# Performance work log

Measured on AMD Instinct MI355X. Metric: run time of the kernel, lower is better.

## Reference

```python
import jax, jax.numpy as jnp
import numpy as np

B, T, C, H = 4, 1024, 1024, 16
D = C // H
EPS = 1e-5


def _ln(x, g, b):
    mu = jnp.mean(x, axis=-1, keepdims=True)
    var = jnp.mean((x - mu) ** 2, axis=-1, keepdims=True)
    return (x - mu) * jax.lax.rsqrt(var + EPS) * g + b


def _attn(xq, xkv, wq, wk, wv, wo, bo, mask):
    # wq/wk/wv/wo: [C, C] (in, out). Dropout is identity in eval mode.
    Bq, Tq, _ = xq.shape
    Tk = xkv.shape[1]
    q = (xq @ wq).reshape(Bq, Tq, H, D)
    k = (xkv @ wk).reshape(Bq, Tk, H, D)
    v = (xkv @ wv).reshape(Bq, Tk, H, D)
    scores = jnp.einsum('bqhd,bkhd->bhqk', q, k) / jnp.sqrt(jnp.float32(D))
    if mask is not None:
        scores = jnp.where(mask == 0, -jnp.inf, scores)
    p = jax.nn.softmax(scores, axis=-1)
    out = jnp.einsum('bhqk,bkhd->bqhd', p, v).reshape(Bq, Tq, C)
    return out @ wo + bo


def setup_inputs() -> dict:
    key = jax.random.key(0)
    ks = jax.random.split(key, 20)
    s = 0.02
    inp = {
        'x': jax.random.normal(ks[0], (B, T, C), jnp.float32),
        'encoder_out': jax.random.normal(ks[1], (B, T, C), jnp.float32),
        'sa_wq': jax.random.normal(ks[2], (C, C), jnp.float32) * s,
        'sa_wk': jax.random.normal(ks[3], (C, C), jnp.float32) * s,
        'sa_wv': jax.random.normal(ks[4], (C, C), jnp.float32) * s,
        'sa_wo': jax.random.normal(ks[5], (C, C), jnp.float32) * s,
        'sa_bo': jnp.zeros((C,), jnp.float32),
        'ca_wq': jax.random.normal(ks[6], (C, C), jnp.float32) * s,
        'ca_wk': jax.random.normal(ks[7], (C, C), jnp.float32) * s,
        'ca_wv': jax.random.normal(ks[8], (C, C), jnp.float32) * s,
        'ca_wo': jax.random.normal(ks[9], (C, C), jnp.float32) * s,
        'ca_bo': jnp.zeros((C,), jnp.float32),
        'ff_w1': jax.random.normal(ks[10], (C, 4 * C), jnp.float32) * s,
        'ff_b1': jnp.zeros((4 * C,), jnp.float32),
        'ff_w2': jax.random.normal(ks[11], (4 * C, C), jnp.float32) * s,
        'ff_b2': jnp.zeros((C,), jnp.float32),
        'ln1_g': jnp.ones((C,), jnp.float32), 'ln1_b': jnp.zeros((C,), jnp.float32),
        'ln2_g': jnp.ones((C,), jnp.float32), 'ln2_b': jnp.zeros((C,), jnp.float32),
        'ln3_g': jnp.ones((C,), jnp.float32), 'ln3_b': jnp.zeros((C,), jnp.float32),
        'tgt_mask': jnp.tril(jnp.ones((T, T), jnp.int32))[None, None],  # [1,1,T,T] causal
        'src_mask': jnp.ones((B, 1, 1, T), jnp.int32),
    }
    return inp


def reference(x, encoder_out, sa_wq, sa_wk, sa_wv, sa_wo, sa_bo,
              ca_wq, ca_wk, ca_wv, ca_wo, ca_bo,
              ff_w1, ff_b1, ff_w2, ff_b2,
              ln1_g, ln1_b, ln2_g, ln2_b, ln3_g, ln3_b,
              tgt_mask, src_mask):
    # self-attention (masked) + residual
    x = x + _attn(_ln(x, ln1_g, ln1_b), _ln(x, ln1_g, ln1_b),
                  sa_wq, sa_wk, sa_wv, sa_wo, sa_bo, tgt_mask)
    # cross-attention + residual (only src_mask applied to scores)
    h = _ln(x, ln2_g, ln2_b)
    x = x + _attn(h, encoder_out, ca_wq, ca_wk, ca_wv, ca_wo, ca_bo, src_mask)
    # FFN + residual
    h = _ln(x, ln3_g, ln3_b)
    x = x + (jax.nn.relu(h @ ff_w1 + ff_b1) @ ff_w2 + ff_b2)
    return x
```

## Files before the change

kernel.cpp:

```cpp
#include <hip/hip_runtime.h>

typedef __bf16 bf16_t;
typedef __bf16 bf16x4 __attribute__((ext_vector_type(4)));
typedef __bf16 bf16x8 __attribute__((ext_vector_type(8)));
typedef float  f32x4  __attribute__((ext_vector_type(4)));

#define LN_EPS 1e-5f

__device__ __forceinline__ void g2l16(const bf16_t* g, bf16_t* l) {
    __builtin_amdgcn_global_load_lds(
        (const __attribute__((address_space(1))) void*)g,
        (__attribute__((address_space(3))) void*)l, 16, 0, 0);
}

__global__ __launch_bounds__(256) void cvt_kernel(
    const float* __restrict__ x, bf16_t* __restrict__ y)
{
    int i = blockIdx.x * 256 + threadIdx.x;
    f32x4 v = ((const f32x4*)x)[i];
    bf16x4 o = { (bf16_t)v.x, (bf16_t)v.y, (bf16_t)v.z, (bf16_t)v.w };
    ((bf16x4*)y)[i] = o;
}

struct WT16 {
    const float* src[16]; bf16_t* dst[16];
    int srcN[16]; int dstK[16]; int k0b[16]; int n0b[16];
};

__global__ __launch_bounds__(256) void wt16_kernel(WT16 p)
{
    const int z = blockIdx.z;
    const float* W = p.src[z];
    bf16_t* Wt = p.dst[z];
    const int N = p.srcN[z], Kd = p.dstK[z];
    const int n0 = p.n0b[z] + blockIdx.x * 64, k0 = p.k0b[z] + blockIdx.y * 64;
    __shared__ float ts[64][65];
    const int tid = threadIdx.x;
#pragma unroll
    for (int it = 0; it < 4; ++it) {
        int f = tid + it * 256;
        int row = f >> 4, c4 = (f & 15) * 4;
        f32x4 v = *(const f32x4*)(W + (size_t)(k0 + row) * N + n0 + c4);
        ts[row][c4 + 0] = v.x; ts[row][c4 + 1] = v.y;
        ts[row][c4 + 2] = v.z; ts[row][c4 + 3] = v.w;
    }
    __syncthreads();
#pragma unroll
    for (int it = 0; it < 4; ++it) {
        int f = tid + it * 256;
        int nrow = f >> 4, k4 = (f & 15) * 4;
        bf16x4 o = { (bf16_t)ts[k4 + 0][nrow], (bf16_t)ts[k4 + 1][nrow],
                     (bf16_t)ts[k4 + 2][nrow], (bf16_t)ts[k4 + 3][nrow] };
        *(bf16x4*)(Wt + (size_t)(n0 + nrow) * Kd + k0 + k4) = o;
    }
}

__global__ __launch_bounds__(256) void ln_kernel(
    const float* __restrict__ x, const float* __restrict__ g,
    const float* __restrict__ b, bf16_t* __restrict__ y)
{
    const int row = blockIdx.x;
    const int tid = threadIdx.x;
    const f32x4* xr = (const f32x4*)(x + (size_t)row * 1024);
    f32x4 v = xr[tid];
    float s  = v.x + v.y + v.z + v.w;
    float s2 = v.x*v.x + v.y*v.y + v.z*v.z + v.w*v.w;
#pragma unroll
    for (int off = 1; off < 64; off <<= 1) {
        s  += __shfl_xor(s,  off, 64);
        s2 += __shfl_xor(s2, off, 64);
    }
    __shared__ float ws_[4], ws2_[4];
    const int wave = tid >> 6, lane = tid & 63;
    if (lane == 0) { ws_[wave] = s; ws2_[wave] = s2; }
    __syncthreads();
    s  = ws_[0] + ws_[1] + ws_[2] + ws_[3];
    s2 = ws2_[0] + ws2_[1] + ws2_[2] + ws2_[3];
    const float mu   = s  * (1.0f/1024.0f);
    const float var  = s2 * (1.0f/1024.0f) - mu*mu;
    const float rstd = rsqrtf(var + LN_EPS);
    f32x4 gv = ((const f32x4*)g)[tid];
    f32x4 bv = ((const f32x4*)b)[tid];
    f32x4 o  = (v - mu) * rstd * gv + bv;
    bf16x4 ob = { (bf16_t)o.x, (bf16_t)o.y, (bf16_t)o.z, (bf16_t)o.w };
    ((bf16x4*)(y + (size_t)row * 1024))[tid] = ob;
}

template<int BN, int DEPTH, int OUT_BF16, int HAS_BIAS, int DO_RELU, int HAS_RES>
__global__ __launch_bounds__(256) void gemm_bf16(
    const bf16_t* __restrict__ A, const bf16_t* __restrict__ Bt,
    const float* __restrict__ bias, const float* __restrict__ res,
    void* __restrict__ out, int M, int N, int K)
{
    constexpr int NT = BN / 32;
    __shared__ __align__(16) bf16_t As[2][DEPTH][128 * 32];
    __shared__ __align__(16) bf16_t Bs[2][DEPTH][BN * 32];

    const int tid  = threadIdx.x;
    const int wave = tid >> 6, lane = tid & 63;
    const int q    = lane >> 4, r = lane & 15;
    const int wm   = wave >> 1, wn = wave & 1;

    const int nbx  = gridDim.x;
    const int id   = blockIdx.y * nbx + blockIdx.x;
    const int mper = gridDim.y >> 3;
    const int jj   = id >> 3;
    const int bm   = (id & 7) * mper + jj / nbx;
    const int bn   = jj % nbx;
    const int m0   = bm * 128, n0 = bn * BN;

    const int srow = lane >> 2;
    const int schk = ((lane & 3) ^ ((lane >> 3) & 3)) * 8;
    const int rsw  = ((r >> 1) & 3) * 8;

    auto stage = [&](int buf, int kk) {
#pragma unroll
        for (int s = 0; s < DEPTH; ++s) {
#pragma unroll
            for (int t = 0; t < 2; ++t) {
                int rowA = wave * 32 + t * 16;
                g2l16(A + (size_t)(m0 + rowA + srow) * K + kk + s * 32 + schk,
                      &As[buf][s][rowA * 32]);
            }
#pragma unroll
            for (int t = 0; t < BN / 64; ++t) {
                int rowB = wave * (BN / 4) + t * 16;
                g2l16(Bt + (size_t)(n0 + rowB + srow) * K + kk + s * 32 + schk,
                      &Bs[buf][s][rowB * 32]);
            }
        }
    };

    f32x4 acc[4][NT] = {};
    constexpr int STEP = 32 * DEPTH;
    stage(0, 0);

    for (int kk = 0; kk < K; kk += STEP) {
        const int cur = (kk / STEP) & 1;
        __syncthreads();
        if (kk + STEP < K) stage(cur ^ 1, kk + STEP);
#pragma unroll
        for (int s = 0; s < DEPTH; ++s) {
            bf16x8 af[4], bfr[NT];
#pragma unroll
            for (int i = 0; i < 4; ++i)
                af[i] = *(const bf16x8*)&As[cur][s][(wm * 64 + i * 16 + r) * 32 + (q * 8 ^ rsw)];
#pragma unroll
            for (int j = 0; j < NT; ++j)
                bfr[j] = *(const bf16x8*)&Bs[cur][s][(wn * 16 * NT + j * 16 + r) * 32 + (q * 8 ^ rsw)];
#pragma unroll
            for (int i = 0; i < 4; ++i)
#pragma unroll
                for (int j = 0; j < NT; ++j)
                    acc[i][j] = __builtin_amdgcn_mfma_f32_16x16x32_bf16(af[i], bfr[j], acc[i][j], 0, 0, 0);
        }
    }

#pragma unroll
    for (int i = 0; i < 4; ++i)
#pragma unroll
        for (int j = 0; j < NT; ++j)
#pragma unroll
            for (int e = 0; e < 4; ++e) {
                int row = m0 + wm * 64 + i * 16 + q * 4 + e;
                int col = n0 + wn * 16 * NT + j * 16 + r;
                float v = acc[i][j][e];
                if (HAS_BIAS) v += bias[col];
                if (DO_RELU)  v = v > 0.0f ? v : 0.0f;
                if (HAS_RES)  v += res[(size_t)row * N + col];
                if (OUT_BF16) ((bf16_t*)out)[(size_t)row * N + col] = (bf16_t)v;
                else          ((float*)out)[(size_t)row * N + col] = v;
            }
}

__global__ __launch_bounds__(256) void gemm_qkv3(
    const bf16_t* __restrict__ Aq, const bf16_t* __restrict__ Akv,
    const bf16_t* __restrict__ Wt3,
    bf16_t* __restrict__ outq, bf16_t* __restrict__ outk,
    bf16_t* __restrict__ vt)
{
    const int K = 1024;
    __shared__ __align__(16) bf16_t As[2][128 * 32];
    __shared__ __align__(16) bf16_t Bs[2][128 * 32];

    const int tid  = threadIdx.x;
    const int wave = tid >> 6, lane = tid & 63;
    const int q    = lane >> 4, r = lane & 15;
    const int wm   = wave >> 1, wn = wave & 1;

    const int nbx  = gridDim.x;
    const int id   = blockIdx.y * nbx + blockIdx.x;
    const int mper = gridDim.y >> 3;
    const int jj   = id >> 3;
    const int bm   = (id & 7) * mper + jj / nbx;
    const int bn   = jj % nbx;
    const int m0   = bm * 128, n0 = bn * 128;
    const int grp  = bn >> 3;
    const bf16_t* A = (grp == 0) ? Aq : Akv;

    const int srow = lane >> 2;
    const int schk = ((lane & 3) ^ ((lane >> 3) & 3)) * 8;
    const int rsw  = ((r >> 1) & 3) * 8;

    auto stage = [&](int buf, int kk) {
#pragma unroll
        for (int t = 0; t < 2; ++t) {
            int row = wave * 32 + t * 16;
            g2l16(A   + (size_t)(m0 + row + srow) * K + kk + schk, &As[buf][row * 32]);
            g2l16(Wt3 + (size_t)(n0 + row + srow) * K + kk + schk, &Bs[buf][row * 32]);
        }
    };

    f32x4 acc[4][4] = {};
    stage(0, 0);

    for (int kk = 0; kk < K; kk += 32) {
        const int cur = (kk >> 5) & 1;
        __syncthreads();
        if (kk + 32 < K) stage(cur ^ 1, kk + 32);

        bf16x8 af[4], bfr[4];
#pragma unroll
        for (int i = 0; i < 4; ++i)
            af[i] = *(const bf16x8*)&As[cur][(wm * 64 + i * 16 + r) * 32 + (q * 8 ^ rsw)];
#pragma unroll
        for (int j = 0; j < 4; ++j)
            bfr[j] = *(const bf16x8*)&Bs[cur][(wn * 64 + j * 16 + r) * 32 + (q * 8 ^ rsw)];
#pragma unroll
        for (int i = 0; i < 4; ++i)
#pragma unroll
            for (int j = 0; j < 4; ++j)
                acc[i][j] = __builtin_amdgcn_mfma_f32_16x16x32_bf16(af[i], bfr[j], acc[i][j], 0, 0, 0);
    }

    if (grp < 2) {
        bf16_t* o = (grp == 0) ? outq : outk;
        const float sc = (grp == 0) ? 0.125f : 1.0f;
        const int c0 = n0 - grp * 1024;
#pragma unroll
        for (int i = 0; i < 4; ++i)
#pragma unroll
            for (int j = 0; j < 4; ++j)
#pragma unroll
                for (int e = 0; e < 4; ++e) {
                    int row = m0 + wm * 64 + i * 16 + q * 4 + e;
                    int col = c0 + wn * 64 + j * 16 + r;
                    o[(size_t)row * 1024 + col] = (bf16_t)(acc[i][j][e] * sc);
                }
    } else {
#pragma unroll
        for (int i = 0; i < 4; ++i)
#pragma unroll
            for (int j = 0; j < 4; ++j) {
                int c = (n0 - 2048) + wn * 64 + j * 16 + r;
                int hh = c >> 6, d = c & 63;
                int row0 = m0 + wm * 64 + i * 16 + q * 4;
                int bb = row0 >> 10, t = row0 & 1023;
                bf16x4 pk = { (bf16_t)acc[i][j][0], (bf16_t)acc[i][j][1],
                              (bf16_t)acc[i][j][2], (bf16_t)acc[i][j][3] };
                *(bf16x4*)&vt[((size_t)((bb << 4) + hh) * 64 + d) * 1024 + t] = pk;
            }
    }
}

template<int CAUSAL>
__global__ __launch_bounds__(256) void attn_mfma_kernel(
    const bf16_t* __restrict__ Qp, const bf16_t* __restrict__ Kp,
    const bf16_t* __restrict__ VTp, bf16_t* __restrict__ Op)
{
    const int T = 1024;
    const int LP = 72;
    __shared__ __align__(16) bf16_t Ps[128 * LP];
    __shared__ __align__(16) bf16_t Ks[2][2][64 * 32];
    __shared__ __align__(16) bf16_t Vs[2][2][64 * 32];

    const int id  = blockIdx.x + 8 * (blockIdx.y + 16 * blockIdx.z);
    int pr, qt;
    if (CAUSAL) {
        const int lo = id & 255;
        pr = lo >> 2;
        const int qp = lo & 3;
        qt = (id >= 256) ? (7 - qp) : qp;
    } else {
        const int jj = id >> 3;
        pr = (id & 7) * 8 + (jj >> 3);
        qt = jj & 7;
    }
    const int h   = pr & 15, b = pr >> 4;

    const int tid  = threadIdx.x;
    const int wave = tid >> 6, lane = tid & 63;
    const int q    = lane >> 4, r = lane & 15;
    const int srow = lane >> 2;
    const int schk = ((lane & 3) ^ ((lane >> 3) & 3)) * 8;
    const int rsw  = ((r >> 1) & 3) * 8;

    const bf16_t* Kb = Kp + (size_t)(b * T) * 1024 + h * 64;
    const bf16_t* Vb = VTp + (size_t)((b * 16 + h) * 64) * 1024;

    auto stageKV = [&](int buf, int kt) {
#pragma unroll
        for (int ks = 0; ks < 2; ++ks) {
            g2l16(Kb + (size_t)(kt * 64 + wave * 16 + srow) * 1024 + ks * 32 + schk,
                  &Ks[buf][ks][wave * 16 * 32]);
            g2l16(Vb + (size_t)(wave * 16 + srow) * 1024 + kt * 64 + ks * 32 + schk,
                  &Vs[buf][ks][wave * 16 * 32]);
        }
    };

    {
        const bf16_t* Qb = Qp + (size_t)(b * T + qt * 128) * 1024 + h * 64;
#pragma unroll
        for (int it = 0; it < 4; ++it) {
            int f = tid + it * 256;
            int row = f >> 3, c8 = (f & 7) * 8;
            *(bf16x8*)&Ps[row * LP + c8] = *(const bf16x8*)(Qb + (size_t)row * 1024 + c8);
        }
    }
    __syncthreads();
    bf16x8 qa[2][2];
#pragma unroll
    for (int mt = 0; mt < 2; ++mt)
#pragma unroll
        for (int ks = 0; ks < 2; ++ks)
            qa[mt][ks] = *(const bf16x8*)&Ps[(wave * 32 + mt * 16 + r) * LP + ks * 32 + q * 8];

    const bf16_t one_b = (bf16_t)1.0f;
    const bf16x8 ones = { one_b, one_b, one_b, one_b, one_b, one_b, one_b, one_b };

    f32x4 o[2][4] = {};
    f32x4 ol[2] = {};

    const int nk = CAUSAL ? (2 * qt + 2) : 16;
    stageKV(0, 0);

    for (int kt = 0; kt < nk; ++kt) {
        const int cur = kt & 1;
        __syncthreads();
        if (kt + 1 < nk) stageKV(cur ^ 1, kt + 1);

        f32x4 s[2][4] = {};
#pragma unroll
        for (int ks = 0; ks < 2; ++ks)
#pragma unroll
            for (int nt = 0; nt < 4; ++nt) {
                bf16x8 kb = *(const bf16x8*)&Ks[cur][ks][(nt * 16 + r) * 32 + (q * 8 ^ rsw)];
#pragma unroll
                for (int mt = 0; mt < 2; ++mt)
                    s[mt][nt] = __builtin_amdgcn_mfma_f32_16x16x32_bf16(qa[mt][ks], kb, s[mt][nt], 0, 0, 0);
            }

        if (CAUSAL) {
#pragma unroll
            for (int mt = 0; mt < 2; ++mt) {
                const int r0 = qt * 128 + wave * 32 + mt * 16;
                if (kt * 64 + 63 > r0) {
#pragma unroll
                    for (int nt = 0; nt < 4; ++nt) {
                        int kg = kt * 64 + nt * 16 + r;
#pragma unroll
                        for (int i2 = 0; i2 < 4; ++i2)
                            if (kg > r0 + q * 4 + i2) s[mt][nt][i2] = -INFINITY;
                    }
                }
            }
        }

#pragma unroll
        for (int mt = 0; mt < 2; ++mt)
#pragma unroll
            for (int nt = 0; nt < 4; ++nt)
#pragma unroll
                for (int i2 = 0; i2 < 4; ++i2)
                    Ps[(wave * 32 + mt * 16 + q * 4 + i2) * LP + nt * 16 + r] =
                        (bf16_t)__expf(s[mt][nt][i2]);

#pragma unroll
        for (int ks = 0; ks < 2; ++ks) {
            bf16x8 pa[2];
#pragma unroll
            for (int mt = 0; mt < 2; ++mt)
                pa[mt] = *(const bf16x8*)&Ps[(wave * 32 + mt * 16 + r) * LP + ks * 32 + q * 8];
#pragma unroll
            for (int dt = 0; dt < 4; ++dt) {
                bf16x8 vb = *(const bf16x8*)&Vs[cur][ks][(dt * 16 + r) * 32 + (q * 8 ^ rsw)];
#pragma unroll
                for (int mt = 0; mt < 2; ++mt)
                    o[mt][dt] = __builtin_amdgcn_mfma_f32_16x16x32_bf16(pa[mt], vb, o[mt][dt], 0, 0, 0);
            }
#pragma unroll
            for (int mt = 0; mt < 2; ++mt)
                ol[mt] = __builtin_amdgcn_mfma_f32_16x16x32_bf16(pa[mt], ones, ol[mt], 0, 0, 0);
        }
    }

    bf16_t* Ob = Op + (size_t)(b * T + qt * 128 + wave * 32) * 1024 + h * 64;
#pragma unroll
    for (int mt = 0; mt < 2; ++mt) {
        f32x4 inv;
#pragma unroll
        for (int i2 = 0; i2 < 4; ++i2) inv[i2] = 1.0f / ol[mt][i2];
#pragma unroll
        for (int dt = 0; dt < 4; ++dt)
#pragma unroll
            for (int i2 = 0; i2 < 4; ++i2)
                Ob[(size_t)(mt * 16 + q * 4 + i2) * 1024 + dt * 16 + r] = (bf16_t)(o[mt][dt][i2] * inv[i2]);
    }
}

extern "C" void kernel_launch(void* const* d_in, const int* in_sizes, int n_in,
                              void* d_out, int out_size, void* d_ws, size_t ws_size,
                              hipStream_t stream)
{
    const float* x     = (const float*)d_in[0];
    const float* enc   = (const float*)d_in[1];
    const float* sa_wq = (const float*)d_in[2];
    const float* sa_wk = (const float*)d_in[3];
    const float* sa_wv = (const float*)d_in[4];
    const float* sa_wo = (const float*)d_in[5];
    const float* sa_bo = (const float*)d_in[6];
    const float* ca_wq = (const float*)d_in[7];
    const float* ca_wk = (const float*)d_in[8];
    const float* ca_wv = (const float*)d_in[9];
    const float* ca_wo = (const float*)d_in[10];
    const float* ca_bo = (const float*)d_in[11];
    const float* ff_w1 = (const float*)d_in[12];
    const float* ff_b1 = (const float*)d_in[13];
    const float* ff_w2 = (const float*)d_in[14];
    const float* ff_b2 = (const float*)d_in[15];
    const float* ln1_g = (const float*)d_in[16];
    const float* ln1_b = (const float*)d_in[17];
    const float* ln2_g = (const float*)d_in[18];
    const float* ln2_b = (const float*)d_in[19];
    const float* ln3_g = (const float*)d_in[20];
    const float* ln3_b = (const float*)d_in[21];

    float* out = (float*)d_out;
    char* ws = (char*)d_ws;
    const size_t MB = 1024 * 1024;
    bf16_t* w_s3  = (bf16_t*)(ws +  0 * MB);
    bf16_t* w_so  = (bf16_t*)(ws +  6 * MB);
    bf16_t* w_c3  = (bf16_t*)(ws +  8 * MB);
    bf16_t* w_co  = (bf16_t*)(ws + 14 * MB);
    bf16_t* w_f1  = (bf16_t*)(ws + 16 * MB);
    bf16_t* w_f2  = (bf16_t*)(ws + 24 * MB);
    bf16_t* b_enc = (bf16_t*)(ws + 32 * MB);
    bf16_t* b_ln  = (bf16_t*)(ws + 40 * MB);
    bf16_t* b_q   = (bf16_t*)(ws + 48 * MB);
    bf16_t* b_k   = (bf16_t*)(ws + 56 * MB);
    bf16_t* b_vt  = (bf16_t*)(ws + 64 * MB);
    bf16_t* b_at  = (bf16_t*)(ws + 72 * MB);
    float*  b_x1  = (float*) (ws + 80 * MB);
    float*  b_x2  = (float*) (ws + 48 * MB);
    bf16_t* b_h1  = (bf16_t*)(ws + 64 * MB);

    const int M = 4096;
    dim3 blk(256);

    WT16 wp;
    const float* srcs[8] = { sa_wq, sa_wk, sa_wv, sa_wo, ca_wq, ca_wk, ca_wv, ca_wo };
    bf16_t* dsts[8] = { w_s3, w_s3 + 1024*1024, w_s3 + 2048*1024, w_so,
                        w_c3, w_c3 + 1024*1024, w_c3 + 2048*1024, w_co };
    for (int z = 0; z < 8; ++z) {
        wp.src[z] = srcs[z]; wp.dst[z] = dsts[z];
        wp.srcN[z] = 1024; wp.dstK[z] = 1024; wp.k0b[z] = 0; wp.n0b[z] = 0;
    }
    for (int z = 8; z < 12; ++z) {
        wp.src[z] = ff_w1; wp.dst[z] = w_f1;
        wp.srcN[z] = 4096; wp.dstK[z] = 1024; wp.k0b[z] = 0; wp.n0b[z] = (z - 8) * 1024;
    }
    for (int z = 12; z < 16; ++z) {
        wp.src[z] = ff_w2; wp.dst[z] = w_f2;
        wp.srcN[z] = 1024; wp.dstK[z] = 4096; wp.k0b[z] = (z - 12) * 1024; wp.n0b[z] = 0;
    }
    wt16_kernel<<<dim3(16, 16, 16), blk, 0, stream>>>(wp);
    cvt_kernel<<<4096, blk, 0, stream>>>(enc, b_enc);

    ln_kernel<<<4096, blk, 0, stream>>>(x, ln1_g, ln1_b, b_ln);
    gemm_qkv3<<<dim3(24, 32), blk, 0, stream>>>(b_ln, b_ln, w_s3, b_q, b_k, b_vt);
    attn_mfma_kernel<1><<<dim3(8, 16, 4), blk, 0, stream>>>(b_q, b_k, b_vt, b_at);
    gemm_bf16<64,2,0,1,0,1><<<dim3(16, 32), blk, 0, stream>>>(
        b_at, w_so, sa_bo, x, b_x1, M, 1024, 1024);
    ln_kernel<<<4096, blk, 0, stream>>>(b_x1, ln2_g, ln2_b, b_ln);
    gemm_qkv3<<<dim3(24, 32), blk, 0, stream>>>(b_ln, b_enc, w_c3, b_q, b_k, b_vt);
    attn_mfma_kernel<0><<<dim3(8, 16, 4), blk, 0, stream>>>(b_q, b_k, b_vt, b_at);
    gemm_bf16<64,2,0,1,0,1><<<dim3(16, 32), blk, 0, stream>>>(
        b_at, w_co, ca_bo, b_x1, b_x2, M, 1024, 1024);
    ln_kernel<<<4096, blk, 0, stream>>>(b_x2, ln3_g, ln3_b, b_ln);
    gemm_bf16<128,1,1,1,1,0><<<dim3(32, 32), blk, 0, stream>>>(
        b_ln, w_f1, ff_b1, nullptr, b_h1, M, 4096, 1024);
    gemm_bf16<64,2,0,1,0,1><<<dim3(16, 32), blk, 0, stream>>>(
        b_h1, w_f2, ff_b2, b_x2, out, M, 1024, 4096);
}
```

Before: 475.2 us.

## Add triple-buffered LDS pipeline with explicit vmcnt waits to BN=64 GEMMs

Adds an NBUF template parameter to the bf16 GEMM. With three buffers, loads are issued two stages ahead, and each iteration waits with an explicit s_waitcnt vmcnt(L) plus a raw barrier instead of __syncthreads. The goal is to keep more global-to-LDS loads in flight and hide memory latency in the output-projection and FFN2 GEMMs. It raises LDS use per block, which may lower occupancy, and it depends on the hand-set vmcnt counts being correct.

```diff
diff --git a/kernel.cpp b/kernel.cpp
--- a/kernel.cpp
+++ b/kernel.cpp
@@ -11,6 +11,21 @@
     __builtin_amdgcn_global_load_lds(
         (const __attribute__((address_space(1))) void*)g,
         (__attribute__((address_space(3))) void*)l, 16, 0, 0);
+}
+
+template<int N> __device__ __forceinline__ void wait_vm() {
+    if constexpr (N == 0)       asm volatile("s_waitcnt vmcnt(0)" ::: "memory");
+    else if constexpr (N == 2)  asm volatile("s_waitcnt vmcnt(2)" ::: "memory");
+    else if constexpr (N == 3)  asm volatile("s_waitcnt vmcnt(3)" ::: "memory");
+    else if constexpr (N == 4)  asm volatile("s_waitcnt vmcnt(4)" ::: "memory");
+    else if constexpr (N == 6)  asm volatile("s_waitcnt vmcnt(6)" ::: "memory");
+    else if constexpr (N == 8)  asm volatile("s_waitcnt vmcnt(8)" ::: "memory");
+    else if constexpr (N == 12) asm volatile("s_waitcnt vmcnt(12)" ::: "memory");
+    else                        asm volatile("s_waitcnt vmcnt(0)" ::: "memory");
+}
+__device__ __forceinline__ void block_bar() {
+    __builtin_amdgcn_s_barrier();
+    asm volatile("" ::: "memory");
 }
 
 __global__ __launch_bounds__(256) void cvt_kernel(
@@ -86,15 +101,17 @@
     ((bf16x4*)(y + (size_t)row * 1024))[tid] = ob;
 }
 
-template<int BN, int DEPTH, int OUT_BF16, int HAS_BIAS, int DO_RELU, int HAS_RES>
+template<int BN, int DEPTH, int NBUF, int OUT_BF16, int HAS_BIAS, int DO_RELU,
+         int HAS_RES>
 __global__ __launch_bounds__(256) void gemm_bf16(
     const bf16_t* __restrict__ A, const bf16_t* __restrict__ Bt,
     const float* __restrict__ bias, const float* __restrict__ res,
     void* __restrict__ out, int M, int N, int K)
 {
     constexpr int NT = BN / 32;
-    __shared__ __align__(16) bf16_t As[2][DEPTH][128 * 32];
-    __shared__ __align__(16) bf16_t Bs[2][DEPTH][BN * 32];
+    constexpr int L  = DEPTH * (2 + BN / 64);
+    __shared__ __align__(16) bf16_t As[NBUF][DEPTH][128 * 32];
+    __shared__ __align__(16) bf16_t Bs[NBUF][DEPTH][BN * 32];
 
     const int tid  = threadIdx.x;
     const int wave = tid >> 6, lane = tid & 63;
@@ -133,27 +150,45 @@
 
     f32x4 acc[4][NT] = {};
     constexpr int STEP = 32 * DEPTH;
-    stage(0, 0);
-
-    for (int kk = 0; kk < K; kk += STEP) {
-        const int cur = (kk / STEP) & 1;
-        __syncthreads();
-        if (kk + STEP < K) stage(cur ^ 1, kk + STEP);
+
+    auto compute = [&](int buf) {
 #pragma unroll
         for (int s = 0; s < DEPTH; ++s) {
             bf16x8 af[4], bfr[NT];
 #pragma unroll
             for (int i = 0; i < 4; ++i)
-                af[i] = *(const bf16x8*)&As[cur][s][(wm * 64 + i * 16 + r) * 32 + (q * 8 ^ rsw)];
+                af[i] = *(const bf16x8*)&As[buf][s][(wm * 64 + i * 16 + r) * 32 + (q * 8 ^ rsw)];
 #pragma unroll
             for (int j = 0; j < NT; ++j)
-                bfr[j] = *(const bf16x8*)&Bs[cur][s][(wn * 16 * NT + j * 16 + r) * 32 + (q * 8 ^ rsw)];
+                bfr[j] = *(const bf16x8*)&Bs[buf][s][(wn * 16 * NT + j * 16 + r) * 32 + (q * 8 ^ rsw)];
 #pragma unroll
             for (int i = 0; i < 4; ++i)
 #pragma unroll
                 for (int j = 0; j < NT; ++j)
                     acc[i][j] = __builtin_amdgcn_mfma_f32_16x16x32_bf16(af[i], bfr[j], acc[i][j], 0, 0, 0);
         }
+    };
+
+    if constexpr (NBUF == 2) {
+        stage(0, 0);
+        for (int kk = 0; kk < K; kk += STEP) {
+            const int cur = (kk / STEP) & 1;
+            __syncthreads();
+            if (kk + STEP < K) stage(cur ^ 1, kk + STEP);
+            compute(cur);
+        }
+    } else {
+        const int NK = K / STEP;
+        stage(0, 0); stage(1, STEP);
+        int t = 0;
+        for (; t + 2 < NK; ++t) {
+            wait_vm<L>();
+            block_bar();
+            stage((t + 2) % NBUF, (t + 2) * STEP);
+            compute(t % NBUF);
+        }
+        wait_vm<L>();  block_bar(); compute(t % NBUF); ++t;
+        wait_vm<0>();  block_bar(); compute(t % NBUF);
     }
 
 #pragma unroll
@@ -479,16 +514,16 @@
     ln_kernel<<<4096, blk, 0, stream>>>(x, ln1_g, ln1_b, b_ln);
     gemm_qkv3<<<dim3(24, 32), blk, 0, stream>>>(b_ln, b_ln, w_s3, b_q, b_k, b_vt);
     attn_mfma_kernel<1><<<dim3(8, 16, 4), blk, 0, stream>>>(b_q, b_k, b_vt, b_at);
-    gemm_bf16<64,2,0,1,0,1><<<dim3(16, 32), blk, 0, stream>>>(
+    gemm_bf16<64,2,3,0,1,0,1><<<dim3(16, 32), blk, 0, stream>>>(
         b_at, w_so, sa_bo, x, b_x1, M, 1024, 1024);
     ln_kernel<<<4096, blk, 0, stream>>>(b_x1, ln2_g, ln2_b, b_ln);
     gemm_qkv3<<<dim3(24, 32), blk, 0, stream>>>(b_ln, b_enc, w_c3, b_q, b_k, b_vt);
     attn_mfma_kernel<0><<<dim3(8, 16, 4), blk, 0, stream>>>(b_q, b_k, b_vt, b_at);
-    gemm_bf16<64,2,0,1,0,1><<<dim3(16, 32), blk, 0, stream>>>(
+    gemm_bf16<64,2,3,0,1,0,1><<<dim3(16, 32), blk, 0, stream>>>(
         b_at, w_co, ca_bo, b_x1, b_x2, M, 1024, 1024);
     ln_kernel<<<4096, blk, 0, stream>>>(b_x2, ln3_g, ln3_b, b_ln);
-    gemm_bf16<128,1,1,1,1,0><<<dim3(32, 32), blk, 0, stream>>>(
+    gemm_bf16<128,1,2,1,1,1,0><<<dim3(32, 32), blk, 0, stream>>>(
         b_ln, w_f1, ff_b1, nullptr, b_h1, M, 4096, 1024);
-    gemm_bf16<64,2,0,1,0,1><<<dim3(16, 32), blk, 0, stream>>>(
+    gemm_bf16<64,2,3,0,1,0,1><<<dim3(16, 32), blk, 0, stream>>>(
         b_h1, w_f2, ff_b2, b_x2, out, M, 1024, 4096);
 }
```

New measurement: 498.2 us. 4.9% more time.

## Add 256x256-tile 512-thread GEMM with quadrant pipelining for FFN up-projection

Applied to the files above, without the earlier changes.

Replaces the 128-tile FFN1 GEMM (bias+ReLU, bf16 out) with a new kernel that computes 256x256 output tiles using 8 waves, K-step 64, XOR-swizzled LDS and double buffering. Each K step is split into four quadrant phases that interleave async global-to-LDS loads of the next tile with MFMA work, using s_setprio and barriers, and block IDs are remapped for L2 locality. Larger tiles raise arithmetic intensity and cut global traffic, but the kernel uses 128KB of LDS and many accumulator registers, so occupancy is one block per CU. The grid is only 256 blocks.

```diff
diff --git a/kernel.cpp b/kernel.cpp
--- a/kernel.cpp
+++ b/kernel.cpp
@@ -171,6 +171,128 @@
                 if (OUT_BF16) ((bf16_t*)out)[(size_t)row * N + col] = (bf16_t)v;
                 else          ((float*)out)[(size_t)row * N + col] = v;
             }
+}
+
+__global__ __launch_bounds__(512) void gemm_256(
+    const bf16_t* __restrict__ A, const bf16_t* __restrict__ Bt,
+    const float* __restrict__ bias, bf16_t* __restrict__ out,
+    int M, int N, int K)
+{
+    __shared__ __align__(16) bf16_t lds[2][2][2][128 * 64];
+
+    const int tid  = threadIdx.x;
+    const int wave = tid >> 6, lane = tid & 63;
+    const int q    = lane >> 4, r = lane & 15;
+    const int wm   = wave >> 2, wn = wave & 3;
+
+    const int id  = blockIdx.y * gridDim.x + blockIdx.x;
+    const int sid = (id & 7) * 32 + (id >> 3);
+    const int bm  = sid >> 4, bn = sid & 15;
+    const int m0  = bm * 256, n0 = bn * 256;
+
+    int srow[2], selem[2];
+#pragma unroll
+    for (int l = 0; l < 2; ++l) {
+        int o  = (wave * 64 + lane) * 16 + l * 8192;
+        int lo = o ^ (((o >> 7) & 7) << 4);
+        srow[l]  = lo >> 7;
+        selem[l] = (lo & 127) >> 1;
+    }
+    const int sd0 = wave * 512;
+
+    auto stageA = [&](int buf, int h, int kt) {
+#pragma unroll
+        for (int l = 0; l < 2; ++l)
+            g2l16(A + (size_t)(m0 + h * 128 + srow[l]) * K + kt * 64 + selem[l],
+                  &lds[buf][0][h][sd0 + l * 4096]);
+    };
+    auto stageB = [&](int buf, int h, int kt) {
+#pragma unroll
+        for (int l = 0; l < 2; ++l)
+            g2l16(Bt + (size_t)(n0 + h * 128 + srow[l]) * K + kt * 64 + selem[l],
+                  &lds[buf][1][h][sd0 + l * 4096]);
+    };
+
+    int aoff[4][2], boff[2][2];
+#pragma unroll
+    for (int i = 0; i < 4; ++i) {
+        int row = wm * 64 + i * 16 + r;
+#pragma unroll
+        for (int ks = 0; ks < 2; ++ks) {
+            int colB = ks * 64 + q * 16;
+            aoff[i][ks] = (row * 128 + (colB ^ ((row & 7) << 4))) >> 1;
+        }
+    }
+#pragma unroll
+    for (int j = 0; j < 2; ++j) {
+        int row = wn * 32 + j * 16 + r;
+#pragma unroll
+        for (int ks = 0; ks < 2; ++ks) {
+            int colB = ks * 64 + q * 16;
+            boff[j][ks] = (row * 128 + (colB ^ ((row & 7) << 4))) >> 1;
+        }
+    }
+
+    f32x4 acc[2][2][4][2] = {};
+
+    stageA(0, 0, 0); stageB(0, 0, 0); stageB(0, 1, 0); stageA(0, 1, 0);
+    asm volatile("s_waitcnt vmcnt(0)" ::: "memory");
+    __builtin_amdgcn_s_barrier();
+    asm volatile("" ::: "memory");
+
+    const int NTk = K >> 6;
+
+#define QPHASE(HA, HB, STMT_STAGE, VMC_ST, VMC_LAST)                           \
+    {                                                                          \
+        bf16x8 af[4][2], bfr[2][2];                                            \
+        _Pragma("unroll") for (int i = 0; i < 4; ++i)                          \
+        _Pragma("unroll") for (int ks = 0; ks < 2; ++ks)                       \
+            af[i][ks] = *(const bf16x8*)&lds[buf][0][HA][aoff[i][ks]];         \
+        _Pragma("unroll") for (int j = 0; j < 2; ++j)                          \
+        _Pragma("unroll") for (int ks = 0; ks < 2; ++ks)                       \
+            bfr[j][ks] = *(const bf16x8*)&lds[buf][1][HB][boff[j][ks]];        \
+        if (st) { STMT_STAGE;                                                  \
+                  asm volatile("s_waitcnt vmcnt(" #VMC_ST ")" ::: "memory"); } \
+        else    { asm volatile("s_waitcnt vmcnt(" #VMC_LAST ")" ::: "memory");}\
+        __builtin_amdgcn_s_barrier();                                          \
+        asm volatile("" ::: "memory");                                         \
+        __builtin_amdgcn_s_setprio(1);                                         \
+        _Pragma("unroll") for (int i = 0; i < 4; ++i)                          \
+        _Pragma("unroll") for (int j = 0; j < 2; ++j)                          \
+        _Pragma("unroll") for (int ks = 0; ks < 2; ++ks)                       \
+            acc[HA][HB][i][j] = __builtin_amdgcn_mfma_f32_16x16x32_bf16(       \
+                af[i][ks], bfr[j][ks], acc[HA][HB][i][j], 0, 0, 0);            \
+        __builtin_amdgcn_s_setprio(0);                                         \
+        __builtin_amdgcn_s_barrier();                                          \
+        asm volatile("" ::: "memory");                                         \
+    }
+
+    for (int kt = 0; kt < NTk; ++kt) {
+        const int buf = kt & 1, nbuf = buf ^ 1;
+        const bool st = (kt + 1 < NTk);
+        QPHASE(0, 0, stageA(nbuf, 0, kt + 1), 4, 2)
+        QPHASE(0, 1, stageB(nbuf, 0, kt + 1), 4, 0)
+        QPHASE(1, 0, stageB(nbuf, 1, kt + 1), 6, 6)
+        QPHASE(1, 1, stageA(nbuf, 1, kt + 1), 4, 6)
+    }
+#undef QPHASE
+
+#pragma unroll
+    for (int hA = 0; hA < 2; ++hA)
+#pragma unroll
+    for (int hB = 0; hB < 2; ++hB)
+#pragma unroll
+    for (int i = 0; i < 4; ++i)
+#pragma unroll
+    for (int j = 0; j < 2; ++j)
+#pragma unroll
+    for (int e = 0; e < 4; ++e) {
+        int row = m0 + hA * 128 + wm * 64 + i * 16 + q * 4 + e;
+        int col = n0 + hB * 128 + wn * 32 + j * 16 + r;
+        float v = acc[hA][hB][i][j][e] + bias[col];
+        v = v > 0.0f ? v : 0.0f;
+        out[(size_t)row * N + col] = (bf16_t)v;
+    }
 }
 
 __global__ __launch_bounds__(256) void gemm_qkv3(
@@ -487,8 +609,8 @@
     gemm_bf16<64,2,0,1,0,1><<<dim3(16, 32), blk, 0, stream>>>(
         b_at, w_co, ca_bo, b_x1, b_x2, M, 1024, 1024);
     ln_kernel<<<4096, blk, 0, stream>>>(b_x2, ln3_g, ln3_b, b_ln);
-    gemm_bf16<128,1,1,1,1,0><<<dim3(32, 32), blk, 0, stream>>>(
-        b_ln, w_f1, ff_b1, nullptr, b_h1, M, 4096, 1024);
+    gemm_256<<<dim3(16, 16), dim3(512), 0, stream>>>(
+        b_ln, w_f1, ff_b1, b_h1, M, 4096, 1024);
     gemm_bf16<64,2,0,1,0,1><<<dim3(16, 32), blk, 0, stream>>>(
         b_h1, w_f2, ff_b2, b_x2, out, M, 1024, 4096);
 }
```

Result: faster. 465.1 us (-2.1%).
